# Kernel tuning notes

Measured on AMD Instinct MI355X. Metric: run time of the kernel, lower is better.

The kernel has to match this reference:

```python
import jax, jax.numpy as jnp
import numpy as np

N, K, D = 500_000, 256, 64  # points, prototypes, feature dim


def setup_inputs() -> dict:
    key = jax.random.key(0)
    kx, km = jax.random.split(key)
    X = jax.random.normal(kx, (N, D), dtype=jnp.float32)
    mus = jax.random.normal(km, (K, D), dtype=jnp.float32)
    return {"X": X, "mus": mus}


def reference(X, mus):
    # Faithful to vmap(lambda x: argmin(sum((mus - x)**2, axis=1)))(X),
    # but expressed with the Gram-matrix distance trick so the K*D broadcast
    # is a single GEMM instead of an O(N,K,D) elementwise intermediate.
    x_sq = jnp.sum(X * X, axis=1, keepdims=True)        # [N, 1]
    mu_sq = jnp.sum(mus * mus, axis=1)                  # [K]
    d2 = x_sq - 2.0 * (X @ mus.T) + mu_sq[None, :]      # [N, K] squared dists
    return jnp.argmin(d2, axis=1)                       # [N] int assignments
```

## Files before the change

kernel.cpp:

```cpp
#include <hip/hip_runtime.h>


#define DIM 64
#define NPROTO 256
#define NBLK 1024
#define MARGIN_ACC 0.017f

using f32x4 = __attribute__((ext_vector_type(4))) float;
using f16x8 = __attribute__((ext_vector_type(8))) _Float16;

__device__ __forceinline__ f16x8 cvt8(float4 a, float4 b) {
    f16x8 r;
    r[0] = (_Float16)a.x; r[1] = (_Float16)a.y;
    r[2] = (_Float16)a.z; r[3] = (_Float16)a.w;
    r[4] = (_Float16)b.x; r[5] = (_Float16)b.y;
    r[6] = (_Float16)b.z; r[7] = (_Float16)b.w;
    return r;
}

__device__ __forceinline__ void barrier_keep_vmcnt() {
    asm volatile("s_waitcnt lgkmcnt(0)" ::: "memory");
    __builtin_amdgcn_s_barrier();
    __builtin_amdgcn_sched_barrier(0);
}

#define PACK_TREE(acc, b1, b2)                                          \
    {                                                                   \
        float pv[4];                                                    \
        _Pragma("unroll")                                               \
        for (int r = 0; r < 4; ++r) {                                   \
            unsigned u = __float_as_uint(acc[r]);                       \
            u = (u & 0xFFFFFF00u) + (unsigned)(kofs - p * 16 - r);      \
            pv[r] = __uint_as_float(u);                                 \
        }                                                               \
        const float t1a = fmaxf(pv[0], pv[1]), t2a = fminf(pv[0], pv[1]);\
        const float t1b = fmaxf(pv[2], pv[3]), t2b = fminf(pv[2], pv[3]);\
        const float p1 = fmaxf(t1a, t1b);                               \
        const float p2 = fmaxf(fminf(t1a, t1b), fmaxf(t2a, t2b));       \
        const float nb2 = fmaxf(fminf(b1, p1), fmaxf(b2, p2));          \
        b1 = fmaxf(b1, p1);                                             \
        b2 = nb2;                                                       \
    }

#define LOADX(gt, x0, x1, x2, x3, y0, y1, y2, y3)                       \
    {                                                                   \
        int rA_ = (gt) * 32 + lp;      rA_ = (rA_ < n) ? rA_ : (n - 1); \
        int rB_ = (gt) * 32 + 16 + lp; rB_ = (rB_ < n) ? rB_ : (n - 1); \
        const float* pA_ = X + (size_t)rA_ * DIM + lg * 8;              \
        const float* pB_ = X + (size_t)rB_ * DIM + lg * 8;              \
        x0 = *(const float4*)(pA_);      x1 = *(const float4*)(pA_ + 4);\
        x2 = *(const float4*)(pA_ + 32); x3 = *(const float4*)(pA_ + 36);\
        y0 = *(const float4*)(pB_);      y1 = *(const float4*)(pB_ + 4);\
        y2 = *(const float4*)(pB_ + 32); y3 = *(const float4*)(pB_ + 36);\
    }

#define BODY(gcur, gnext, PAR, x0, x1, x2, x3, y0, y1, y2, y3)          \
    {                                                                   \
        const f16x8 bxA0 = cvt8(x0, x1), bxA1 = cvt8(x2, x3);           \
        const f16x8 bxB0 = cvt8(y0, y1), bxB1 = cvt8(y2, y3);           \
        LOADX(gnext, x0, x1, x2, x3, y0, y1, y2, y3)                    \
        float b1A = -3.4e38f, b2A = -3.4e38f;                           \
        float b1B = -3.4e38f, b2B = -3.4e38f;                           \
        _Pragma("unroll")                                               \
        for (int p = 0; p < 8; ++p) {                                   \
            const f32x4 seed = *(const f32x4*)&s_seed[sbase + p * 16];  \
            f32x4 accA = __builtin_amdgcn_mfma_f32_16x16x32_f16(        \
                ah[p][0], bxA0, seed, 0, 0, 0);                         \
            f32x4 accB = __builtin_amdgcn_mfma_f32_16x16x32_f16(        \
                ah[p][0], bxB0, seed, 0, 0, 0);                         \
            accA = __builtin_amdgcn_mfma_f32_16x16x32_f16(              \
                ah[p][1], bxA1, accA, 0, 0, 0);                         \
            accB = __builtin_amdgcn_mfma_f32_16x16x32_f16(              \
                ah[p][1], bxB1, accB, 0, 0, 0);                         \
            PACK_TREE(accA, b1A, b2A)                                   \
            PACK_TREE(accB, b1B, b2B)                                   \
        }                                                               \
        _Pragma("unroll")                                               \
        for (int m = 16; m <= 32; m <<= 1) {                            \
            const float o1A = __shfl_xor(b1A, m), o2A = __shfl_xor(b2A, m);\
            const float o1B = __shfl_xor(b1B, m), o2B = __shfl_xor(b2B, m);\
            const float n2A = fmaxf(fminf(b1A, o1A), fmaxf(b2A, o2A));  \
            const float n2B = fmaxf(fminf(b1B, o1B), fmaxf(b2B, o2B));  \
            b1A = fmaxf(b1A, o1A); b2A = n2A;                           \
            b1B = fmaxf(b1B, o1B); b2B = n2B;                           \
        }                                                               \
         \
         \
        if (w == 0 && l >= 16 && l < 32)                                \
            s_pair[PAR][0][l] = make_uint2(__float_as_uint(b1B),        \
                                           __float_as_uint(b2B));       \
        if (w == 1 && l < 16)                                           \
            s_pair[PAR][1][l] = make_uint2(__float_as_uint(b1A),        \
                                           __float_as_uint(b2A));       \
        barrier_keep_vmcnt();                                           \
        const bool mine = (w == 0) ? (l < 16) : (l >= 16 && l < 32);    \
        if (mine) {                                                     \
            float f1 = (l < 16) ? b1A : b1B;                            \
            float f2 = (l < 16) ? b2A : b2B;                            \
            const uint2 o = s_pair[PAR][1 - w][l];                      \
            const float o1 = __uint_as_float(o.x);                      \
            const float o2 = __uint_as_float(o.y);                      \
            const float nb2 = fmaxf(fminf(f1, o1), fmaxf(f2, o2));      \
            f1 = fmaxf(f1, o1);                                         \
            f2 = nb2;                                                   \
            const int i = (gcur) * 32 + l;                              \
            if (i < n) {                                                \
                const unsigned u1 = __float_as_uint(f1);                \
                const int k1 = 255 - (int)(u1 & 0xFFu);                 \
                const float v1 = __uint_as_float(u1 & 0xFFFFFF00u);     \
                const float v2 =                                        \
                    __uint_as_float(__float_as_uint(f2) & 0xFFFFFF00u); \
                const unsigned fb =                                     \
                    ((v1 - v2) < MARGIN_ACC) ? 0x80000000u : 0u;        \
                out[i] = (int)((unsigned)k1 | fb);                      \
            }                                                           \
        }                                                               \
    }

__attribute__((amdgpu_waves_per_eu(2, 4)))
__global__ void __launch_bounds__(128)
argmin_mfma_kernel(const float* __restrict__ X,
                   const float* __restrict__ mus,
                   int* __restrict__ out, int n) {
    __shared__ __align__(16) float s_seed[NPROTO];
    __shared__ uint2 s_pair[2][2][32];

    const int tid = threadIdx.x;
    const int w = tid >> 6;
    const int l = tid & 63;
    const int lp = l & 15;
    const int lg = l >> 4;

    f16x8 ah[8][2];
#pragma unroll
    for (int p = 0; p < 8; ++p) {
        const float* src = mus + (size_t)(w * 128 + p * 16 + lp) * DIM + lg * 8;
        const float4 a = *(const float4*)(src);
        const float4 b = *(const float4*)(src + 4);
        const float4 c = *(const float4*)(src + 32);
        const float4 d = *(const float4*)(src + 36);
        ah[p][0] = cvt8(a, b);
        ah[p][1] = cvt8(c, d);
        float s = 0.f;
        s = fmaf(a.x, a.x, fmaf(a.y, a.y, fmaf(a.z, a.z, fmaf(a.w, a.w, s))));
        s = fmaf(b.x, b.x, fmaf(b.y, b.y, fmaf(b.z, b.z, fmaf(b.w, b.w, s))));
        s = fmaf(c.x, c.x, fmaf(c.y, c.y, fmaf(c.z, c.z, fmaf(c.w, c.w, s))));
        s = fmaf(d.x, d.x, fmaf(d.y, d.y, fmaf(d.z, d.z, fmaf(d.w, d.w, s))));
        s += __shfl_xor(s, 16);
        s += __shfl_xor(s, 32);
        if (lg == 0) s_seed[w * 128 + p * 16 + lp] = -0.5f * s;
    }
    __syncthreads();

    const int ng2 = (n + 31) / 32;
    const int q = ng2 / NBLK, rr = ng2 % NBLK;
    const int bid = blockIdx.x;
    const int g0 = bid * q + (bid < rr ? bid : rr);
    const int cnt = q + (bid < rr ? 1 : 0);
    const int glast = g0 + cnt - 1;

    const int kofs = 255 - w * 128 - lg * 4;
    const int sbase = w * 128 + lg * 4;

    float4 pa0, pa1, pa2, pa3, pb0, pb1, pb2, pb3;
    float4 qa0, qa1, qa2, qa3, qb0, qb1, qb2, qb3;
    LOADX(g0, pa0, pa1, pa2, pa3, pb0, pb1, pb2, pb3)
    {
        const int g1 = (g0 + 1 < glast) ? (g0 + 1) : glast;
        LOADX(g1, qa0, qa1, qa2, qa3, qb0, qb1, qb2, qb3)
    }

    int it = 0;
    for (; it + 1 < cnt; it += 2) {
        const int gA = g0 + it;
        const int gB = g0 + it + 1;
        const int nA = (gA + 2 < glast) ? (gA + 2) : glast;
        const int nB = (gB + 2 < glast) ? (gB + 2) : glast;
        BODY(gA, nA, 0, pa0, pa1, pa2, pa3, pb0, pb1, pb2, pb3)
        BODY(gB, nB, 1, qa0, qa1, qa2, qa3, qb0, qb1, qb2, qb3)
    }
    if (it < cnt) {
        const int gA = g0 + it;
        BODY(gA, glast, 0, pa0, pa1, pa2, pa3, pb0, pb1, pb2, pb3)
    }
}

#define MSTRIDE 65

__global__ void __launch_bounds__(256)
fixup_scan_lds_kernel(const float* __restrict__ X,
                      const float* __restrict__ mus,
                      int* __restrict__ out, int n) {
    __shared__ float s_mu[NPROTO * MSTRIDE];
    __shared__ float s_msq[NPROTO];

    const int tid = threadIdx.x;
    {
        const float4* mr = (const float4*)(mus + (size_t)tid * DIM);
        float q0 = 0.f, q1 = 0.f, q2 = 0.f, q3 = 0.f;
#pragma unroll
        for (int qq = 0; qq < 16; ++qq) {
            const float4 mv = mr[qq];
            const int base = tid * MSTRIDE + qq * 4;
            s_mu[base]     = mv.x;
            s_mu[base + 1] = mv.y;
            s_mu[base + 2] = mv.z;
            s_mu[base + 3] = mv.w;
            q0 = fmaf(mv.x, mv.x, q0);
            q1 = fmaf(mv.y, mv.y, q1);
            q2 = fmaf(mv.z, mv.z, q2);
            q3 = fmaf(mv.w, mv.w, q3);
        }
        s_msq[tid] = (q0 + q1) + (q2 + q3);
    }
    __syncthreads();

    const int l = tid & 63;
    const int gw = (int)((blockIdx.x * blockDim.x + tid) >> 6);
    const int NW = (int)((gridDim.x * blockDim.x) >> 6);
    const int chunk = (n + NW - 1) / NW;
    const int base = gw * chunk;
    const int end = (base + chunk < n) ? (base + chunk) : n;

    for (int s = base; s < end; s += 64) {
        const int i = s + l;
        const int v = (i < end) ? out[i] : 0;
        const bool flg = (i < end) && ((unsigned)v & 0x80000000u);
        unsigned long long m = __ballot(flg);
        while (m) {
            const int src = (int)__ffsll((unsigned long long)m) - 1;
            m &= m - 1;
            const int pt = __shfl(i, src);
            const float4* xr = (const float4*)(X + (size_t)pt * DIM);
            float4 xv[16];
            float a0 = 0.f, a1 = 0.f, a2 = 0.f, a3 = 0.f;
#pragma unroll
            for (int qq = 0; qq < 16; ++qq) {
                xv[qq] = xr[qq];
                a0 = fmaf(xv[qq].x, xv[qq].x, a0);
                a1 = fmaf(xv[qq].y, xv[qq].y, a1);
                a2 = fmaf(xv[qq].z, xv[qq].z, a2);
                a3 = fmaf(xv[qq].w, xv[qq].w, a3);
            }
            const float xsq = (a0 + a1) + (a2 + a3);
            float b1 = 3.4e38f;
            int k1 = 0;
#pragma unroll
            for (int e = 0; e < 4; ++e) {
                const int p = e * 64 + l;
                const float* mr = &s_mu[p * MSTRIDE];
                float d0 = 0.f, d1 = 0.f, d2 = 0.f, d3 = 0.f;
#pragma unroll
                for (int qq = 0; qq < 16; ++qq) {
                    d0 = fmaf(mr[qq * 4],     xv[qq].x, d0);
                    d1 = fmaf(mr[qq * 4 + 1], xv[qq].y, d1);
                    d2 = fmaf(mr[qq * 4 + 2], xv[qq].z, d2);
                    d3 = fmaf(mr[qq * 4 + 3], xv[qq].w, d3);
                }
                const float dot = (d0 + d1) + (d2 + d3);
                const float dd = (xsq - 2.0f * dot) + s_msq[p];
                if (dd < b1) { b1 = dd; k1 = p; }
            }
#pragma unroll
            for (int mm = 1; mm < 64; mm <<= 1) {
                const float ob = __shfl_xor(b1, mm);
                const int ok = __shfl_xor(k1, mm);
                if (ob < b1 || (ob == b1 && ok < k1)) { b1 = ob; k1 = ok; }
            }
            if (l == 0) out[pt] = k1;
        }
    }
}

extern "C" void kernel_launch(void* const* d_in, const int* in_sizes, int n_in,
                              void* d_out, int out_size, void* d_ws, size_t ws_size,
                              hipStream_t stream) {
    const float* X = (const float*)d_in[0];
    const float* mus = (const float*)d_in[1];
    int* out = (int*)d_out;
    const int n = in_sizes[0] / DIM;

    argmin_mfma_kernel<<<NBLK, 128, 0, stream>>>(X, mus, out, n);
    fixup_scan_lds_kernel<<<512, 256, 0, stream>>>(X, mus, out, n);
}
```

Baseline: 89.74 us.

## Compact ambiguous points into a workspace list for targeted fp32 fixup

The MFMA pass now appends indices of points whose top-two distance margin is small to a global list in workspace, using a wave ballot plus one atomic per wave. The fixup kernel then walks only that list instead of scanning all N outputs for flag bits. This removes the full scan of the output array, at the cost of a memset launch, atomics, and a scattered list read. The old scan path is kept as a fallback when the workspace is too small.

```diff
diff --git a/kernel.cpp b/kernel.cpp
--- a/kernel.cpp
+++ b/kernel.cpp
@@ -94,7 +94,9 @@
                                            __float_as_uint(b2A));       \
         barrier_keep_vmcnt();                                           \
         const bool mine = (w == 0) ? (l < 16) : (l >= 16 && l < 32);    \
-        if (mine) {                                                     \
+        bool fl = false;                                                \
+        const int i = (gcur) * 32 + l;                                  \
+        if (mine && i < n) {                                            \
             float f1 = (l < 16) ? b1A : b1B;                            \
             float f2 = (l < 16) ? b2A : b2B;                            \
             const uint2 o = s_pair[PAR][1 - w][l];                      \
@@ -103,16 +105,31 @@
             const float nb2 = fmaxf(fminf(f1, o1), fmaxf(f2, o2));      \
             f1 = fmaxf(f1, o1);                                         \
             f2 = nb2;                                                   \
-            const int i = (gcur) * 32 + l;                              \
-            if (i < n) {                                                \
-                const unsigned u1 = __float_as_uint(f1);                \
-                const int k1 = 255 - (int)(u1 & 0xFFu);                 \
-                const float v1 = __uint_as_float(u1 & 0xFFFFFF00u);     \
-                const float v2 =                                        \
-                    __uint_as_float(__float_as_uint(f2) & 0xFFFFFF00u); \
-                const unsigned fb =                                     \
-                    ((v1 - v2) < MARGIN_ACC) ? 0x80000000u : 0u;        \
-                out[i] = (int)((unsigned)k1 | fb);                      \
+            const unsigned u1 = __float_as_uint(f1);                    \
+            const int k1 = 255 - (int)(u1 & 0xFFu);                     \
+            const float v1 = __uint_as_float(u1 & 0xFFFFFF00u);         \
+            const float v2 =                                            \
+                __uint_as_float(__float_as_uint(f2) & 0xFFFFFF00u);     \
+            const bool close = (v1 - v2) < MARGIN_ACC;                  \
+            if (use_list) {                                             \
+                out[i] = k1;                                            \
+                fl = close;                                             \
+            } else {                                                    \
+                out[i] = (int)((unsigned)k1 |                           \
+                               (close ? 0x80000000u : 0u));             \
+            }                                                           \
+        }                                                               \
+        if (use_list) {                                                 \
+            const unsigned long long mask = __ballot(fl);               \
+            if (mask) {                                                 \
+                unsigned base = 0;                                      \
+                if (l == 0)                                             \
+                    base = atomicAdd(ws_count,                          \
+                                     (unsigned)__popcll(mask));         \
+                base = __shfl(base, 0);                                 \
+                if (fl)                                                 \
+                    ws_list[base +                                      \
+                            __popcll(mask & ((1ull << l) - 1))] = i;    \
             }                                                           \
         }                                                               \
     }
@@ -121,7 +138,10 @@
 __global__ void __launch_bounds__(128)
 argmin_mfma_kernel(const float* __restrict__ X,
                    const float* __restrict__ mus,
-                   int* __restrict__ out, int n) {
+                   int* __restrict__ out,
+                   unsigned* __restrict__ ws_count,
+                   int* __restrict__ ws_list,
+                   int use_list, int n) {
     __shared__ __align__(16) float s_seed[NPROTO];
     __shared__ uint2 s_pair[2][2][32];
 
@@ -188,6 +208,81 @@
 #define MSTRIDE 65
 
 __global__ void __launch_bounds__(256)
+fixup_lds_kernel(const float* __restrict__ X, const float* __restrict__ mus,
+                 const unsigned* __restrict__ ws_count,
+                 const int* __restrict__ ws_list, int* __restrict__ out) {
+    __shared__ float s_mu[NPROTO * MSTRIDE];
+    __shared__ float s_msq[NPROTO];
+
+    const int tid = threadIdx.x;
+    {
+        const float4* mr = (const float4*)(mus + (size_t)tid * DIM);
+        float q0 = 0.f, q1 = 0.f, q2 = 0.f, q3 = 0.f;
+#pragma unroll
+        for (int qq = 0; qq < 16; ++qq) {
+            const float4 mv = mr[qq];
+            const int base = tid * MSTRIDE + qq * 4;
+            s_mu[base]     = mv.x;
+            s_mu[base + 1] = mv.y;
+            s_mu[base + 2] = mv.z;
+            s_mu[base + 3] = mv.w;
+            q0 = fmaf(mv.x, mv.x, q0);
+            q1 = fmaf(mv.y, mv.y, q1);
+            q2 = fmaf(mv.z, mv.z, q2);
+            q3 = fmaf(mv.w, mv.w, q3);
+        }
+        s_msq[tid] = (q0 + q1) + (q2 + q3);
+    }
+    __syncthreads();
+
+    const int l = tid & 63;
+    const int gw = (int)((blockIdx.x * blockDim.x + tid) >> 6);
+    const int NW = (int)((gridDim.x * blockDim.x) >> 6);
+    const int nf = (int)*ws_count;
+
+    for (int j = gw; j < nf; j += NW) {
+        const int pt = ws_list[j];
+        const float4* xr = (const float4*)(X + (size_t)pt * DIM);
+        float4 xv[16];
+        float a0 = 0.f, a1 = 0.f, a2 = 0.f, a3 = 0.f;
+#pragma unroll
+        for (int qq = 0; qq < 16; ++qq) {
+            xv[qq] = xr[qq];
+            a0 = fmaf(xv[qq].x, xv[qq].x, a0);
+            a1 = fmaf(xv[qq].y, xv[qq].y, a1);
+            a2 = fmaf(xv[qq].z, xv[qq].z, a2);
+            a3 = fmaf(xv[qq].w, xv[qq].w, a3);
+        }
+        const float xsq = (a0 + a1) + (a2 + a3);
+        float b1 = 3.4e38f;
+        int k1 = 0;
+#pragma unroll
+        for (int e = 0; e < 4; ++e) {
+            const int p = e * 64 + l;
+            const float* mr = &s_mu[p * MSTRIDE];
+            float d0 = 0.f, d1 = 0.f, d2 = 0.f, d3 = 0.f;
+#pragma unroll
+            for (int qq = 0; qq < 16; ++qq) {
+                d0 = fmaf(mr[qq * 4],     xv[qq].x, d0);
+                d1 = fmaf(mr[qq * 4 + 1], xv[qq].y, d1);
+                d2 = fmaf(mr[qq * 4 + 2], xv[qq].z, d2);
+                d3 = fmaf(mr[qq * 4 + 3], xv[qq].w, d3);
+            }
+            const float dot = (d0 + d1) + (d2 + d3);
+            const float dd = (xsq - 2.0f * dot) + s_msq[p];
+            if (dd < b1) { b1 = dd; k1 = p; }
+        }
+#pragma unroll
+        for (int mm = 1; mm < 64; mm <<= 1) {
+            const float ob = __shfl_xor(b1, mm);
+            const int ok = __shfl_xor(k1, mm);
+            if (ob < b1 || (ob == b1 && ok < k1)) { b1 = ob; k1 = ok; }
+        }
+        if (l == 0) out[pt] = k1;
+    }
+}
+
+__global__ void __launch_bounds__(256)
 fixup_scan_lds_kernel(const float* __restrict__ X,
                       const float* __restrict__ mus,
                       int* __restrict__ out, int n) {
@@ -280,6 +375,20 @@
     int* out = (int*)d_out;
     const int n = in_sizes[0] / DIM;
 
-    argmin_mfma_kernel<<<NBLK, 128, 0, stream>>>(X, mus, out, n);
-    fixup_scan_lds_kernel<<<512, 256, 0, stream>>>(X, mus, out, n);
-}
+    unsigned* ws_count = (unsigned*)d_ws;
+    int* ws_list = (int*)((char*)d_ws + 16);
+    const int use_list = (ws_size >= 16 + (size_t)n * 4) ? 1 : 0;
+
+    if (use_list) {
+        hipMemsetAsync(d_ws, 0, 16, stream);
+    }
+
+    argmin_mfma_kernel<<<NBLK, 128, 0, stream>>>(X, mus, out, ws_count,
+                                                 ws_list, use_list, n);
+    if (use_list) {
+        fixup_lds_kernel<<<512, 256, 0, stream>>>(X, mus, ws_count, ws_list,
+                                                  out);
+    } else {
+        fixup_scan_lds_kernel<<<512, 256, 0, stream>>>(X, mus, out, n);
+    }
+}
```

Measured after the change: 81.22 us. 9.5% less time.
